# Kernel tuning notes

Hardware: AMD Instinct MI355X
Metric: run time of the kernel (lower is better)

## Reference

```python
import jax, jax.numpy as jnp
import numpy as np

N_QUBITS = 6
N_LAYERS = 6
DIM = 2 ** N_QUBITS  # 64


def _qft_matrix():
    # PennyLane qml.QFT matrix: F[j,k] = exp(2*pi*i*j*k/N) / sqrt(N)
    j = np.arange(DIM)
    F = np.exp(2j * np.pi * np.outer(j, j) / DIM) / np.sqrt(DIM)
    return jnp.asarray(F, dtype=jnp.complex64)


def _cnot_ring_perm():
    # Composite permutation of basis states for CNOT(q, (q+1)%n) applied q=0..n-1.
    # Wire 0 is the most significant bit (PennyLane convention).
    m = np.arange(DIM)
    for q in range(N_QUBITS):
        c_bit = N_QUBITS - 1 - q
        t_bit = N_QUBITS - 1 - ((q + 1) % N_QUBITS)
        ctrl = (m >> c_bit) & 1
        m = np.where(ctrl == 1, m ^ (1 << t_bit), m)
    # state_out[m_final] = state_in[m_init]  ->  gather index = argsort(m)
    return jnp.asarray(np.argsort(m), dtype=jnp.int32)


_QFT = _qft_matrix()
_CNOT_PERM = _cnot_ring_perm()


def _layer_unitary(thetas):
    # kron of per-qubit RY(theta) gates (they act on distinct wires -> single 64x64 matrix)
    c = jnp.cos(thetas / 2.0)
    s = jnp.sin(thetas / 2.0)
    U = jnp.array(1.0, dtype=thetas.dtype).reshape(1, 1)
    for q in range(N_QUBITS):
        g = jnp.stack([jnp.stack([c[q], -s[q]]), jnp.stack([s[q], c[q]])])  # [2,2]
        U = jnp.kron(U, g)
    return U.astype(jnp.complex64)  # [64,64]


def setup_inputs() -> dict:
    key = jax.random.key(0)
    k1, k2 = jax.random.split(key)
    x = jax.random.normal(k1, (65536, DIM), dtype=jnp.float32)
    weights_rot = jax.random.normal(k2, (N_LAYERS, N_QUBITS), dtype=jnp.float32) * 0.01
    return {"x": x, "weights_rot": weights_rot}


def reference(x, weights_rot):
    # AmplitudeEmbedding with normalize=True
    norm = jnp.sqrt(jnp.sum(x * x, axis=-1, keepdims=True))
    psi = (x / norm).astype(jnp.complex64)  # [B, 64]
    # QFT on all wires
    psi = jnp.einsum('jk,bk->bj', _QFT, psi)
    # layers: fused RY-on-all-wires unitary, then CNOT ring permutation
    for l in range(N_LAYERS):
        U = _layer_unitary(weights_rot[l])
        psi = jnp.einsum('ij,bj->bi', U, psi)
        psi = jnp.take(psi, _CNOT_PERM, axis=1)
    # probs over all wires
    return psi.real ** 2 + psi.imag ** 2  # [B, 64] float32
```

## Files before the change

kernel.cpp:

```cpp
#include <hip/hip_runtime.h>
#include <hip/hip_bf16.h>

#define NQ 6
#define DIM 64
#define NLAYERS 6

typedef __attribute__((ext_vector_type(8))) short bf16x8;
typedef __attribute__((ext_vector_type(4))) float f32x4;

#define GLOAD_LDS16(gp, lp) \
    __builtin_amdgcn_global_load_lds((const __attribute__((address_space(1))) void*)(gp), \
                                     (__attribute__((address_space(3))) void*)(lp), 16, 0, 0)

__global__ __launch_bounds__(64) void build_M(const float* __restrict__ w,
                                              unsigned short* __restrict__ Bf) {
    const int k = blockIdx.x;
    const int j = threadIdx.x;

    int t = (j * k) & 63;
    float sv, cv;
    __sincosf((float)t * (3.14159265358979f / 32.0f), &sv, &cv);
    float vr = cv * 0.125f;
    float vi = sv * 0.125f;

    int m = j;
#pragma unroll
    for (int q = 0; q < NQ; ++q) {
        int cb = 5 - q;
        int tb = 5 - ((q + 1) % NQ);
        if ((m >> cb) & 1) m ^= (1 << tb);
    }
    const int dst4 = m << 2;

#pragma unroll
    for (int l = 0; l < NLAYERS; ++l) {
#pragma unroll
        for (int q = 0; q < NQ; ++q) {
            float th = w[l * NQ + q] * 0.5f;
            float c = __cosf(th), s = __sinf(th);
            int b = 5 - q;
            float pr = __shfl_xor(vr, 1 << b);
            float pi = __shfl_xor(vi, 1 << b);
            float sgn = ((j >> b) & 1) ? s : -s;
            vr = c * vr + sgn * pr;
            vi = c * vi + sgn * pi;
        }
        vr = __int_as_float(__builtin_amdgcn_ds_permute(dst4, __float_as_int(vr)));
        vi = __int_as_float(__builtin_amdgcn_ds_permute(dst4, __float_as_int(vi)));
    }

    const int jt = j >> 4;
    const int lane16 = (j & 15) + 16 * ((k >> 3) & 3);
    const int chunk = k >> 5;
    const int e = k & 7;
    const int base = ((jt * 2 + chunk) * 2) * 512 + lane16 * 8 + e;

    __hip_bfloat16 rh = __float2bfloat16(vr);
    __hip_bfloat16 ih = __float2bfloat16(vi);
    Bf[base]       = *(unsigned short*)&rh;
    Bf[base + 512] = *(unsigned short*)&ih;
}

__global__ __launch_bounds__(1024) void qenc_main(const float* __restrict__ x,
                                                  const unsigned short* __restrict__ Bf,
                                                  float* __restrict__ out) {
    __shared__ __align__(16) unsigned short sB[8192];
    const int tid = threadIdx.x;
    const int lane = tid & 63;
    const int wid = tid >> 6;
    const int row0 = blockIdx.x * 256 + wid * 16;
    const int r = lane & 15;
    const int g = lane >> 4;

    const float* xp = x + (size_t)(row0 + r) * DIM + 8 * g;
    float4 va = *(const float4*)(xp);
    float4 vb = *(const float4*)(xp + 4);
    float4 vc = *(const float4*)(xp + 32);
    float4 vd = *(const float4*)(xp + 36);

    GLOAD_LDS16(Bf + (size_t)tid * 8, sB + (size_t)tid * 8);

    float xf[16];
    *(float4*)(xf)      = va;  *(float4*)(xf + 4)  = vb;
    *(float4*)(xf + 8)  = vc;  *(float4*)(xf + 12) = vd;

    float n0 = 0.f;
#pragma unroll
    for (int i = 0; i < 16; ++i) n0 = fmaf(xf[i], xf[i], n0);
    n0 += __shfl_xor(n0, 16);
    n0 += __shfl_xor(n0, 32);
    const float inv = 1.0f / n0;

    bf16x8 xh[2], xl[2];
#pragma unroll
    for (int c = 0; c < 2; ++c)
#pragma unroll
        for (int i = 0; i < 8; ++i) {
            float f = xf[c * 8 + i];
            __hip_bfloat16 hh = __float2bfloat16(f);
            __hip_bfloat16 ll = __float2bfloat16(f - __bfloat162float(hh));
            xh[c][i] = *(short*)&hh;
            xl[c][i] = *(short*)&ll;
        }

    __syncthreads();

    const f32x4 z = {0.f, 0.f, 0.f, 0.f};
    f32x4 acr[4] = {z, z, z, z};
    f32x4 aci[4] = {z, z, z, z};
    const unsigned short* bp = sB + lane * 8;

#pragma unroll
    for (int jt = 0; jt < 4; ++jt) {
#pragma unroll
        for (int c = 0; c < 2; ++c) {
            const unsigned short* fb = bp + ((jt * 2 + c) * 2) * 512;
            bf16x8 mr = *(const bf16x8*)(fb);
            bf16x8 mi = *(const bf16x8*)(fb + 512);
            acr[jt] = __builtin_amdgcn_mfma_f32_16x16x32_bf16(mr, xh[c], acr[jt], 0, 0, 0);
            acr[jt] = __builtin_amdgcn_mfma_f32_16x16x32_bf16(mr, xl[c], acr[jt], 0, 0, 0);
            aci[jt] = __builtin_amdgcn_mfma_f32_16x16x32_bf16(mi, xh[c], aci[jt], 0, 0, 0);
            aci[jt] = __builtin_amdgcn_mfma_f32_16x16x32_bf16(mi, xl[c], aci[jt], 0, 0, 0);
        }
    }

    float* op = out + (size_t)(row0 + r) * DIM + 4 * g;
#pragma unroll
    for (int jt = 0; jt < 4; ++jt) {
        float4 o;
        o.x = (acr[jt][0] * acr[jt][0] + aci[jt][0] * aci[jt][0]) * inv;
        o.y = (acr[jt][1] * acr[jt][1] + aci[jt][1] * aci[jt][1]) * inv;
        o.z = (acr[jt][2] * acr[jt][2] + aci[jt][2] * aci[jt][2]) * inv;
        o.w = (acr[jt][3] * acr[jt][3] + aci[jt][3] * aci[jt][3]) * inv;
        *(float4*)(op + jt * 16) = o;
    }
}

extern "C" void kernel_launch(void* const* d_in, const int* in_sizes, int n_in,
                              void* d_out, int out_size, void* d_ws, size_t ws_size,
                              hipStream_t stream) {
    const float* x = (const float*)d_in[0];
    const float* w = (const float*)d_in[1];
    float* out = (float*)d_out;
    unsigned short* Bf = (unsigned short*)d_ws;
    int B = in_sizes[0] / DIM;

    hipLaunchKernelGGL(build_M, dim3(DIM), dim3(64), 0, stream, w, Bf);
    hipLaunchKernelGGL(qenc_main, dim3(B / 256), dim3(1024), 0, stream, x, Bf, out);
}
```

Baseline: 17.11 us.

## Load fused unitary fragments directly into registers, drop LDS staging and sync

The main kernel no longer stages the 16 KB bf16 matrix in LDS with global_load_lds and a block barrier. Each wave now loads its 16 MFMA B-fragments straight from global memory (L2-resident) into registers. Blocks shrink from 1024 to 256 threads with more blocks launched, which removes the __syncthreads stall and the LDS footprint. In exchange every wave issues its own 16 KB of matrix loads and uses more VGPRs.

```diff
diff --git a/kernel.cpp b/kernel.cpp
--- a/kernel.cpp
+++ b/kernel.cpp
@@ -7,10 +7,6 @@
 
 typedef __attribute__((ext_vector_type(8))) short bf16x8;
 typedef __attribute__((ext_vector_type(4))) float f32x4;
-
-#define GLOAD_LDS16(gp, lp) \
-    __builtin_amdgcn_global_load_lds((const __attribute__((address_space(1))) void*)(gp), \
-                                     (__attribute__((address_space(3))) void*)(lp), 16, 0, 0)
 
 __global__ __launch_bounds__(64) void build_M(const float* __restrict__ w,
                                               unsigned short* __restrict__ Bf) {
@@ -61,28 +57,30 @@
     Bf[base + 512] = *(unsigned short*)&ih;
 }
 
-__global__ __launch_bounds__(1024) void qenc_main(const float* __restrict__ x,
-                                                  const unsigned short* __restrict__ Bf,
-                                                  float* __restrict__ out) {
-    __shared__ __align__(16) unsigned short sB[8192];
+__global__ __launch_bounds__(256, 4) void qenc_main(const float* __restrict__ x,
+                                                    const unsigned short* __restrict__ Bf,
+                                                    float* __restrict__ out) {
     const int tid = threadIdx.x;
     const int lane = tid & 63;
     const int wid = tid >> 6;
-    const int row0 = blockIdx.x * 256 + wid * 16;
+    const int row0 = blockIdx.x * 64 + wid * 16;
     const int r = lane & 15;
     const int g = lane >> 4;
 
+    const bf16x8* bb = (const bf16x8*)Bf + lane;
+    bf16x8 mfr[8], mfi[8];
+#pragma unroll
+    for (int f = 0; f < 8; ++f) {
+        mfr[f] = bb[(f * 2 + 0) * 64];
+        mfi[f] = bb[(f * 2 + 1) * 64];
+    }
+
     const float* xp = x + (size_t)(row0 + r) * DIM + 8 * g;
-    float4 va = *(const float4*)(xp);
-    float4 vb = *(const float4*)(xp + 4);
-    float4 vc = *(const float4*)(xp + 32);
-    float4 vd = *(const float4*)(xp + 36);
-
-    GLOAD_LDS16(Bf + (size_t)tid * 8, sB + (size_t)tid * 8);
-
     float xf[16];
-    *(float4*)(xf)      = va;  *(float4*)(xf + 4)  = vb;
-    *(float4*)(xf + 8)  = vc;  *(float4*)(xf + 12) = vd;
+    *(float4*)(xf)      = *(const float4*)(xp);
+    *(float4*)(xf + 4)  = *(const float4*)(xp + 4);
+    *(float4*)(xf + 8)  = *(const float4*)(xp + 32);
+    *(float4*)(xf + 12) = *(const float4*)(xp + 36);
 
     float n0 = 0.f;
 #pragma unroll
@@ -103,24 +101,18 @@
             xl[c][i] = *(short*)&ll;
         }
 
-    __syncthreads();
-
     const f32x4 z = {0.f, 0.f, 0.f, 0.f};
     f32x4 acr[4] = {z, z, z, z};
     f32x4 aci[4] = {z, z, z, z};
-    const unsigned short* bp = sB + lane * 8;
-
 #pragma unroll
     for (int jt = 0; jt < 4; ++jt) {
 #pragma unroll
         for (int c = 0; c < 2; ++c) {
-            const unsigned short* fb = bp + ((jt * 2 + c) * 2) * 512;
-            bf16x8 mr = *(const bf16x8*)(fb);
-            bf16x8 mi = *(const bf16x8*)(fb + 512);
-            acr[jt] = __builtin_amdgcn_mfma_f32_16x16x32_bf16(mr, xh[c], acr[jt], 0, 0, 0);
-            acr[jt] = __builtin_amdgcn_mfma_f32_16x16x32_bf16(mr, xl[c], acr[jt], 0, 0, 0);
-            aci[jt] = __builtin_amdgcn_mfma_f32_16x16x32_bf16(mi, xh[c], aci[jt], 0, 0, 0);
-            aci[jt] = __builtin_amdgcn_mfma_f32_16x16x32_bf16(mi, xl[c], aci[jt], 0, 0, 0);
+            const int f = jt * 2 + c;
+            acr[jt] = __builtin_amdgcn_mfma_f32_16x16x32_bf16(mfr[f], xh[c], acr[jt], 0, 0, 0);
+            acr[jt] = __builtin_amdgcn_mfma_f32_16x16x32_bf16(mfr[f], xl[c], acr[jt], 0, 0, 0);
+            aci[jt] = __builtin_amdgcn_mfma_f32_16x16x32_bf16(mfi[f], xh[c], aci[jt], 0, 0, 0);
+            aci[jt] = __builtin_amdgcn_mfma_f32_16x16x32_bf16(mfi[f], xl[c], aci[jt], 0, 0, 0);
         }
     }
 
@@ -146,5 +138,5 @@
     int B = in_sizes[0] / DIM;
 
     hipLaunchKernelGGL(build_M, dim3(DIM), dim3(64), 0, stream, w, Bf);
-    hipLaunchKernelGGL(qenc_main, dim3(B / 256), dim3(1024), 0, stream, x, Bf, out);
+    hipLaunchKernelGGL(qenc_main, dim3(B / 64), dim3(256), 0, stream, x, Bf, out);
 }
```

New measurement: 18.93 us. 1.11x slower.
